# Optimization experiments

Measured on AMD Instinct MI355X. Metric: run time of the kernel, lower is better.

## Reference

```python
import jax, jax.numpy as jnp
import numpy as np

N = 1024          # num_features
H = N // 2        # core dimension (num_params // 2)
NB = 4            # num_blocks
B = 16384         # batch


def _lifted_core(rot_params, diag_params):
    """Build the (N, N) lifted core matrix for one Cayley block."""
    # skew-symmetric matrix from the H rotation params
    S = rot_params[:, None] - rot_params[None, :]            # (H, H)
    I = jnp.eye(H, dtype=rot_params.dtype)
    rotation = jnp.linalg.solve(I - S, I + S)                # Cayley transform
    core = diag_params[:, None] * rotation                   # diag(d) @ rotation
    # rot90(core, k=o) only depends on o mod 4 -> precompute 4 variants
    rots = jnp.stack([core,
                      jnp.rot90(core, 1),
                      jnp.rot90(core, 2),
                      jnp.rot90(core, 3)])                   # (4, H, H)

    def body(lifted, o):
        blk = jax.lax.dynamic_slice(lifted, (o, o), (H, H)) + rots[o % 4]
        return jax.lax.dynamic_update_slice(lifted, blk, (o, o)), None

    lifted, _ = jax.lax.scan(body, jnp.zeros((N, N), dtype=core.dtype),
                             jnp.arange(H + 1))
    return lifted


def setup_inputs() -> dict:
    key = jax.random.key(0)
    ks = jax.random.split(key, 5)
    x = jax.random.normal(ks[0], (B, N), dtype=jnp.float32)
    enc_rot = jax.random.normal(ks[1], (NB, H), dtype=jnp.float32)
    enc_diag = jax.random.normal(ks[2], (NB, H), dtype=jnp.float32)
    dec_rot = jax.random.normal(ks[3], (NB, H), dtype=jnp.float32)
    dec_diag = jax.random.normal(ks[4], (NB, H), dtype=jnp.float32)
    return {"x": x, "enc_rot": enc_rot, "enc_diag": enc_diag,
            "dec_rot": dec_rot, "dec_diag": dec_diag}


def reference(x, enc_rot, enc_diag, dec_rot, dec_diag):
    s = x
    for i in range(NB):                                      # encoder blocks
        s = s @ _lifted_core(enc_rot[i], enc_diag[i]).T
    bottleneck = s
    out = s
    for i in range(NB):                                      # decoder blocks
        out = out @ _lifted_core(dec_rot[i], dec_diag[i]).T
    return bottleneck, out
```

## Files before the change

kernel.cpp:

```cpp
#include <hip/hip_runtime.h>
#include <hip/hip_bf16.h>
#include <cstdint>
#include <cstddef>

#define H 512
#define NFEAT 1024
#define BATCH 16384
#define LM ((size_t)1 << 20)

using bf16 = __hip_bfloat16;
using bf16x8 = __attribute__((ext_vector_type(8))) __bf16;
using f32x4 = __attribute__((ext_vector_type(4))) float;
using f32x16 = __attribute__((ext_vector_type(16))) float;

__device__ __forceinline__ void gload16(void* lds, const void* g) {
  __builtin_amdgcn_global_load_lds(
      (__attribute__((address_space(1))) void*)g,
      (__attribute__((address_space(3))) void*)lds,
      16, 0, 0);
}

__global__ void prep_kernel(const float* __restrict__ er, const float* __restrict__ ed,
                            const float* __restrict__ dr, const float* __restrict__ dd,
                            float* __restrict__ ab) {
  const int mat = blockIdx.x;
  const int lane = threadIdx.x;
  const float* u = (mat < 4) ? (er + mat * H) : (dr + (mat - 4) * H);
  const float* d = (mat < 4) ? (ed + mat * H) : (dd + (mat - 4) * H);

  double s = 0.0, q = 0.0;
  for (int k = 0; k < 8; ++k) {
    double v = (double)u[lane + 64 * k];
    s += v;
    q += v * v;
  }
  for (int off = 32; off; off >>= 1) {
    s += __shfl_down(s, off);
    q += __shfl_down(q, off);
  }
  s = __shfl(s, 0);
  q = __shfl(q, 0);

  const double det = 1.0 - s * s + (double)H * q;
  const double cuv = 2.0 * (1.0 + s) / det;
  const double cuu = -2.0 * (double)H / det;
  const double cvv = -2.0 * q / det;
  const double cvu = -2.0 * (1.0 - s) / det;

  float* a = ab + mat * 1024;
  float* b = a + H;
  for (int k = 0; k < 8; ++k) {
    int idx = lane + 64 * k;
    double ui = (double)u[idx], di = (double)d[idx];
    a[idx] = (float)(di * (cuv * ui + cvv));
    b[idx] = (float)(di * (cuu * ui + cvu));
  }
}

__global__ __launch_bounds__(256) void prep2_kernel(
    const float* __restrict__ er, const float* __restrict__ ed,
    const float* __restrict__ dr, const float* __restrict__ dd,
    const float* __restrict__ ab, float* __restrict__ Tpref) {
  __shared__ float buf[4][512];
  __shared__ float tmp[4][512];
  const int mat = blockIdx.x;
  const float* d = (mat < 4) ? (ed + mat * H) : (dd + (mat - 4) * H);
  const float* a = ab + mat * 1024;
  const int t = threadIdx.x;
  for (int m = t; m < 512; m += 256) {
    buf[0][m] = a[m];
    buf[1][m] = a[511 - m];
    buf[2][m] = d[m];
    buf[3][m] = d[511 - m];
  }
  __syncthreads();
  for (int s = 4; s <= 256; s <<= 1) {
    for (int m = t; m < 512; m += 256)
#pragma unroll
      for (int q = 0; q < 4; ++q) tmp[q][m] = (m >= s) ? buf[q][m - s] : 0.f;
    __syncthreads();
    for (int m = t; m < 512; m += 256)
#pragma unroll
      for (int q = 0; q < 4; ++q) buf[q][m] += tmp[q][m];
    __syncthreads();
  }
  float* tp = Tpref + mat * 2048;
  for (int m = t; m < 512; m += 256) {
    tp[m] = buf[0][m];
    tp[512 + m] = buf[1][m];
    tp[1024 + m] = buf[2][m];
    tp[1536 + m] = buf[3][m];
  }
}

__global__ __launch_bounds__(256) void build_kernel(
    const float* __restrict__ er, const float* __restrict__ ed,
    const float* __restrict__ dr, const float* __restrict__ dd,
    const float* __restrict__ ab, const float* __restrict__ Tpref,
    bf16* __restrict__ Lbase) {
  __shared__ __align__(16) float arr4[4][520];
  __shared__ __align__(16) float4 up[132];
  __shared__ float pa[512], parev[512], pd[512], pdrev[512], sdl[512];

  const int i = blockIdx.x;
  const int mat = blockIdx.y;
  const float* u = (mat < 4) ? (er + mat * H) : (dr + (mat - 4) * H);
  const float* d = (mat < 4) ? (ed + mat * H) : (dd + (mat - 4) * H);
  const float* a = ab + mat * 1024;
  const float* b = a + H;
  const float* tp = Tpref + mat * 2048;
  const int t = threadIdx.x;

  for (int m = t; m < 520; m += 256) {
    arr4[0][m] = (m < 512) ? u[m] : 0.f;
    arr4[1][m] = (m >= 1 && m <= 512) ? b[m - 1] : 0.f;
    arr4[2][m] = (m >= 2 && m <= 513) ? u[513 - m] : 0.f;
    arr4[3][m] = (m >= 3 && m <= 514) ? b[514 - m] : 0.f;
  }
  for (int m = t; m < 512; m += 256) {
    pa[m] = tp[m];
    parev[m] = tp[512 + m];
    pd[m] = tp[1024 + m];
    pdrev[m] = tp[1536 + m];
    sdl[m] = d[m];
  }
  if (t < 132) {
    const int k4 = 4 * t;
    float4 v;
    int p0 = i - k4;
    v.x = (p0 >= 0 && p0 < 512) ? b[p0] : 0.f;
    int p1 = i - k4 - 1;
    v.y = (p1 >= 0 && p1 < 512) ? u[511 - p1] : 0.f;
    int p2 = i - k4 - 2;
    v.z = (p2 >= 0 && p2 < 512) ? b[511 - p2] : 0.f;
    int p3 = i - k4 - 3;
    v.w = (p3 >= 0 && p3 < 512) ? u[p3] : 0.f;
    up[t] = v;
  }
  __syncthreads();

  const float* upf = (const float*)up;
  const int j0 = t * 4;

  int lo_[4], hi_[4];
#pragma unroll
  for (int c = 0; c < 4; ++c) {
    const int jc = j0 + c;
    lo_[c] = max(0, max(i, jc) - 511);
    hi_[c] = min(512, min(i, jc));
  }
  const int CL = lo_[3];
  const int CH = hi_[0];

  float acc[4] = {0.f, 0.f, 0.f, 0.f};

#pragma unroll
  for (int c = 0; c < 4; ++c) {
    const int jc = j0 + c;
    const int lo = lo_[c], hi = hi_[c];
    if (lo > hi) continue;
    float v = 0.f;
    {
      int o1 = lo + ((0 - lo) & 3), o2 = hi - ((hi - 0) & 3);
      if (o1 <= o2) { int mx = i - o1, mn = i - o2; v += pa[mx] - (mn >= 4 ? pa[mn - 4] : 0.f); }
    }
    {
      int o1 = lo + ((1 - lo) & 3), o2 = hi - ((hi - 1) & 3);
      if (o1 <= o2) { int mx = jc - o1, mn = jc - o2; v += pa[mx] - (mn >= 4 ? pa[mn - 4] : 0.f); }
    }
    {
      int o1 = lo + ((2 - lo) & 3), o2 = hi - ((hi - 2) & 3);
      if (o1 <= o2) { int mx = i - o1, mn = i - o2; v += parev[mx] - (mn >= 4 ? parev[mn - 4] : 0.f); }
    }
    {
      int o1 = lo + ((3 - lo) & 3), o2 = hi - ((hi - 3) & 3);
      if (o1 <= o2) { int mx = jc - o1, mn = jc - o2; v += parev[mx] - (mn >= 4 ? parev[mn - 4] : 0.f); }
    }
    if (i == jc) {
      {
        int o1 = lo + ((0 - lo) & 3), o2 = hi - ((hi - 0) & 3);
        if (o1 <= o2) { int mx = i - o1, mn = i - o2; v += pd[mx] - (mn >= 4 ? pd[mn - 4] : 0.f); }
      }
      {
        int o1 = lo + ((2 - lo) & 3), o2 = hi - ((hi - 2) & 3);
        if (o1 <= o2) { int mx = i - o1, mn = i - o2; v += pdrev[mx] - (mn >= 4 ? pdrev[mn - 4] : 0.f); }
      }
    }
    const int m2 = i + jc - 511;
    if (m2 >= 0 && !(m2 & 1)) {
      const int os = m2 >> 1;
      if (os >= lo && os <= hi) {
        const int r = os & 3;
        if (r == 1) v += sdl[jc - os];
        else if (r == 3) v += sdl[511 - (jc - os)];
      }
    }
    acc[c] = v;
  }

  if (CL > CH) {
#pragma unroll
    for (int c = 0; c < 4; ++c) {
      const int jc = j0 + c;
      for (int o = lo_[c]; o <= hi_[c]; ++o) {
        const int r = o & 3;
        acc[c] += upf[o] * arr4[r][jc - o + r];
      }
    }
  } else {
#pragma unroll
    for (int c = 0; c < 4; ++c) {
      const int jc = j0 + c;
      const int he = min(hi_[c], CL - 1);
      for (int o = lo_[c]; o <= he; ++o) {
        const int r = o & 3;
        acc[c] += upf[o] * arr4[r][jc - o + r];
      }
      const int ls = max(lo_[c], CH + 1);
      for (int o = ls; o <= hi_[c]; ++o) {
        const int r = o & 3;
        acc[c] += upf[o] * arr4[r][jc - o + r];
      }
    }
    const int QL = (CL + 3) & ~3;
    for (int o = CL; o < QL && o <= CH; ++o) {
      const int r = o & 3;
      const float uvv = upf[o];
      const float4 wv = *(const float4*)&arr4[r][j0 - o + r];
      acc[0] += uvv * wv.x; acc[1] += uvv * wv.y;
      acc[2] += uvv * wv.z; acc[3] += uvv * wv.w;
    }
    int ob = QL;
    for (; ob + 3 <= CH; ob += 4) {
      const float4 uv = up[ob >> 2];
      const int x = j0 - ob;
      const float4 w0 = *(const float4*)&arr4[0][x];
      const float4 w1 = *(const float4*)&arr4[1][x];
      const float4 w2 = *(const float4*)&arr4[2][x];
      const float4 w3 = *(const float4*)&arr4[3][x];
      acc[0] += uv.x * w0.x + uv.y * w1.x + uv.z * w2.x + uv.w * w3.x;
      acc[1] += uv.x * w0.y + uv.y * w1.y + uv.z * w2.y + uv.w * w3.y;
      acc[2] += uv.x * w0.z + uv.y * w1.z + uv.z * w2.z + uv.w * w3.z;
      acc[3] += uv.x * w0.w + uv.y * w1.w + uv.z * w2.w + uv.w * w3.w;
    }
    for (int o = ob; o <= CH; ++o) {
      const int r = o & 3;
      const float uvv = upf[o];
      const float4 wv = *(const float4*)&arr4[r][j0 - o + r];
      acc[0] += uvv * wv.x; acc[1] += uvv * wv.y;
      acc[2] += uvv * wv.z; acc[3] += uvv * wv.w;
    }
  }

  const size_t off = ((size_t)mat << 21) + ((size_t)i << 10) + (size_t)j0;
  union { bf16 v[4]; ushort4 s; } Hu, Lu;
#pragma unroll
  for (int c = 0; c < 4; ++c) {
    const bf16 hb = __float2bfloat16(acc[c]);
    Hu.v[c] = hb;
    Lu.v[c] = __float2bfloat16(acc[c] - __bfloat162float(hb));
  }
  *(ushort4*)(Lbase + off) = Hu.s;
  *(ushort4*)(Lbase + off + LM) = Lu.s;
}

__global__ void splith_kernel(const float* __restrict__ x, bf16* __restrict__ h) {
  const int n4 = BATCH * NFEAT / 4;
  int idx = blockIdx.x * blockDim.x + threadIdx.x;
  int stride = gridDim.x * blockDim.x;
  for (int i = idx; i < n4; i += stride) {
    float4 v = ((const float4*)x)[i];
    union { bf16 b[4]; short4 s; } Hu;
    Hu.b[0] = __float2bfloat16(v.x);
    Hu.b[1] = __float2bfloat16(v.y);
    Hu.b[2] = __float2bfloat16(v.z);
    Hu.b[3] = __float2bfloat16(v.w);
    ((short4*)h)[i] = Hu.s;
  }
}

struct TPtrs { const bf16* s; bf16* d; };
struct T6 { TPtrs t[6]; };

__global__ __launch_bounds__(256) void transposeB_kernel(T6 p) {
  const bf16* S = p.t[blockIdx.z].s;
  bf16* D = p.t[blockIdx.z].d;
  __shared__ ushort tile[64][68];
  const int i0 = blockIdx.x * 64, j0 = blockIdx.y * 64;
  const int tid = threadIdx.x;
  const int rr = tid >> 4;
  const int cc = (tid & 15) * 4;
#pragma unroll
  for (int it = 0; it < 4; ++it) {
    const int row = it * 16 + rr;
    const size_t so = (size_t)(i0 + row) * 1024 + j0 + cc;
    ushort4 v = *(const ushort4*)((const ushort*)S + so);
    tile[row][cc] = v.x; tile[row][cc + 1] = v.y;
    tile[row][cc + 2] = v.z; tile[row][cc + 3] = v.w;
  }
  __syncthreads();
#pragma unroll
  for (int it = 0; it < 4; ++it) {
    const int row = it * 16 + rr;
    ushort4 o;
    o.x = tile[cc][row];     o.y = tile[cc + 1][row];
    o.z = tile[cc + 2][row]; o.w = tile[cc + 3][row];
    const size_t dofs = (size_t)(j0 + row) * 1024 + i0 + cc;
    *(ushort4*)((ushort*)D + dofs) = o;
  }
}

struct GPtrs { const bf16* a; const bf16* b; bf16* yh; bf16* yl; };
struct G4 { GPtrs g[4]; };

__global__ __launch_bounds__(256) void chaingemm4_kernel(G4 p) {
  GPtrs q = p.g[blockIdx.z];
  const bf16* A = q.a;
  const bf16* Bh = q.b;
  const bf16* Bl = q.b + LM;

  __shared__ __align__(16) bf16 smem[2 * 3 * 4096];

  const int tid = threadIdx.x;
  const int lane = tid & 63;
  const int wave = tid >> 6;
  const int wr = wave >> 1, wc = wave & 1;
  const int r0 = blockIdx.x * 64, c0 = blockIdx.y * 64;

  const int srow = tid >> 3;
  const int scol = (((tid & 7) ^ (srow & 7))) * 8;
  const int dst = tid * 8;
  const size_t ga0 = (size_t)(r0 + srow) * 1024 + scol;
  const size_t gb0 = (size_t)(c0 + srow) * 1024 + scol;

  auto STAGE = [&](int nb, int k0) {
    bf16* base = smem + nb * 12288;
    gload16(base + dst,        A + ga0 + k0);
    gload16(base + 2048 + dst, A + ga0 + 32 * 1024 + k0);
    gload16(base + 4096 + dst,        Bh + gb0 + k0);
    gload16(base + 4096 + 2048 + dst, Bh + gb0 + 32 * 1024 + k0);
    gload16(base + 8192 + dst,        Bl + gb0 + k0);
    gload16(base + 8192 + 2048 + dst, Bl + gb0 + 32 * 1024 + k0);
  };

  const int l31 = lane & 31;
  const int klg = lane >> 5;
  const int ar = wr * 32 + l31;
  const int br = wc * 32 + l31;
  int aoff[4], boff[4];
#pragma unroll
  for (int ks = 0; ks < 4; ++ks) {
    const int lgA = (ks << 1) | klg;
    aoff[ks] = ar * 64 + ((lgA ^ (ar & 7)) << 3);
    boff[ks] = br * 64 + ((lgA ^ (br & 7)) << 3);
  }

  f32x16 acc = {};

  STAGE(0, 0);
  asm volatile("s_waitcnt vmcnt(0)" ::: "memory");
  __builtin_amdgcn_s_barrier();

  for (int t = 0; t < 16; ++t) {
    const int buf = t & 1;
    const int nb = buf ^ 1;
    const bool pf = (t < 15);
    if (pf) STAGE(nb, (t + 1) * 64);

    const bf16* pA = smem + buf * 12288;
    const bf16* pBh = pA + 4096;
    const bf16* pBl = pA + 8192;
#pragma unroll
    for (int ks = 0; ks < 4; ++ks) {
      bf16x8 ah = *(const bf16x8*)(pA + aoff[ks]);
      bf16x8 bh = *(const bf16x8*)(pBh + boff[ks]);
      bf16x8 bl = *(const bf16x8*)(pBl + boff[ks]);
      acc = __builtin_amdgcn_mfma_f32_32x32x16_bf16(ah, bh, acc, 0, 0, 0);
      acc = __builtin_amdgcn_mfma_f32_32x32x16_bf16(ah, bl, acc, 0, 0, 0);
    }
    if (pf) asm volatile("s_waitcnt vmcnt(0)" ::: "memory");
    __builtin_amdgcn_s_barrier();
  }

  const int oc = c0 + wc * 32 + l31;
  const int rb = (lane >> 5) << 2;
#pragma unroll
  for (int r = 0; r < 16; ++r) {
    const int gr = r0 + wr * 32 + (r & 3) + ((r >> 2) << 3) + rb;
    const size_t off = (size_t)gr * 1024 + oc;
    const float v = acc[r];
    const bf16 hb = __float2bfloat16(v);
    q.yh[off] = hb;
    q.yl[off] = __float2bfloat16(v - __bfloat162float(hb));
  }
}

__global__ __launch_bounds__(512, 1) void gemmbig_kernel(
    const bf16* __restrict__ A, const bf16* __restrict__ Bh_,
    float* __restrict__ Y0, float* __restrict__ Y1) {
  __shared__ __align__(16) bf16 smem[2 * 2 * 8192];

  const int tid = threadIdx.x;
  const int lane = tid & 63;
  const int wave = tid >> 6;
  const int wr = wave >> 2;
  const int wc = wave & 3;

  const int pdisp = blockIdx.x + (blockIdx.y << 6);
  const int xcd = pdisp & 7;
  const int chk = pdisp >> 3;
  const int row0 = (xcd * 8 + (chk >> 3)) * 256;
  const int col0 = (chk & 7) * 256;

  const int gsrc = (tid & 3) ^ ((tid >> 3) & 3);
  const int dst = tid * 8;
  const size_t abase = (size_t)(row0 + (tid >> 2)) * NFEAT + gsrc * 8;
  const size_t bbase = (size_t)(col0 + (tid >> 2)) * NFEAT + gsrc * 8;

  auto STAGE2 = [&](int nb, int arr, const bf16* __restrict__ src, size_t base, int k0) {
    bf16* d = smem + nb * 16384 + arr * 8192 + dst;
    gload16(d, src + base + k0);
    gload16(d + 4096, src + base + 131072 + k0);
  };

  const int l31 = lane & 31;
  const int hb = lane >> 5;
  int aoffB[4][2], boffB[2][2];
#pragma unroll
  for (int m = 0; m < 4; ++m) {
    const int r = wr * 128 + m * 32 + l31;
#pragma unroll
    for (int ks = 0; ks < 2; ++ks)
      aoffB[m][ks] = r * 64 + ((((ks << 1) | hb) ^ ((r >> 1) & 3)) << 4);
  }
#pragma unroll
  for (int n = 0; n < 2; ++n) {
    const int r = wc * 64 + n * 32 + l31;
#pragma unroll
    for (int ks = 0; ks < 2; ++ks)
      boffB[n][ks] = r * 64 + ((((ks << 1) | hb) ^ ((r >> 1) & 3)) << 4);
  }

  auto LD = [](const char* base, int off) { return *(const bf16x8*)(base + off); };

  f32x16 acc[4][2] = {};

  STAGE2(0, 0, A, abase, 0);
  STAGE2(0, 1, Bh_, bbase, 0);
  asm volatile("s_waitcnt vmcnt(0)" ::: "memory");
  __builtin_amdgcn_s_barrier();

  for (int t = 0; t < 32; ++t) {
    const int buf = t & 1;
    const int nb = buf ^ 1;
    const int k1 = (t + 1) * 32;
    const char* pA = (const char*)(smem + buf * 16384);
    const char* pBh = pA + 16384;
    const bool pf = (t < 31);

    bf16x8 ga[2][2], fbh[2][2];

    if (pf) {
      STAGE2(nb, 0, A, abase, k1);
      STAGE2(nb, 1, Bh_, bbase, k1);
    }
#pragma unroll
    for (int mi = 0; mi < 2; ++mi)
#pragma unroll
      for (int ks = 0; ks < 2; ++ks)
        ga[mi][ks] = LD(pA, aoffB[mi][ks]);
#pragma unroll
    for (int n = 0; n < 2; ++n)
#pragma unroll
      for (int ks = 0; ks < 2; ++ks)
        fbh[n][ks] = LD(pBh, boffB[n][ks]);
    __builtin_amdgcn_s_barrier();
    __builtin_amdgcn_s_setprio(1);
#pragma unroll
    for (int ks = 0; ks < 2; ++ks)
#pragma unroll
      for (int mi = 0; mi < 2; ++mi)
#pragma unroll
        for (int n = 0; n < 2; ++n)
          acc[mi][n] = __builtin_amdgcn_mfma_f32_32x32x16_bf16(ga[mi][ks], fbh[n][ks], acc[mi][n], 0, 0, 0);
    __builtin_amdgcn_s_setprio(0);
    __builtin_amdgcn_s_barrier();

#pragma unroll
    for (int mi = 0; mi < 2; ++mi)
#pragma unroll
      for (int ks = 0; ks < 2; ++ks)
        ga[mi][ks] = LD(pA, aoffB[2 + mi][ks]);
    __builtin_amdgcn_s_barrier();
    __builtin_amdgcn_s_setprio(1);
#pragma unroll
    for (int ks = 0; ks < 2; ++ks)
#pragma unroll
      for (int mi = 0; mi < 2; ++mi)
#pragma unroll
        for (int n = 0; n < 2; ++n)
          acc[2 + mi][n] = __builtin_amdgcn_mfma_f32_32x32x16_bf16(ga[mi][ks], fbh[n][ks], acc[2 + mi][n], 0, 0, 0);
    __builtin_amdgcn_s_setprio(0);
    if (pf) asm volatile("s_waitcnt vmcnt(0)" ::: "memory");
    __builtin_amdgcn_s_barrier();
  }

  float* Yb = (col0 < 1024) ? Y0 : (Y1 - 1024);
  const int ocol0 = col0 + wc * 64 + l31;
  const int rb = (lane >> 5) << 2;
#pragma unroll
  for (int m = 0; m < 4; ++m)
#pragma unroll
    for (int n = 0; n < 2; ++n)
#pragma unroll
      for (int r = 0; r < 16; ++r) {
        const int grow = row0 + wr * 128 + m * 32 + (r & 3) + ((r >> 2) << 3) + rb;
        const int gcol = ocol0 + n * 32;
        Yb[(size_t)grow * NFEAT + (size_t)gcol] = acc[m][n][r];
      }
}

extern "C" void kernel_launch(void* const* d_in, const int* in_sizes, int n_in,
                              void* d_out, int out_size, void* d_ws, size_t ws_size,
                              hipStream_t stream) {
  (void)in_sizes; (void)n_in; (void)out_size; (void)ws_size;
  const float* x  = (const float*)d_in[0];
  const float* er = (const float*)d_in[1];
  const float* ed = (const float*)d_in[2];
  const float* dr = (const float*)d_in[3];
  const float* dd = (const float*)d_in[4];

  float* O0 = (float*)d_out;
  float* O1 = O0 + (size_t)BATCH * NFEAT;

  bf16* Lb = (bf16*)d_ws;
  float* ab = (float*)(Lb + 16 * LM);
  bf16* Qh = (bf16*)(ab + 8 * 1024);

  float* Tpref = O0;
  bf16* SB = (bf16*)((char*)O0 + (1 << 20));
  auto slot = [&](int s) { return SB + (size_t)s * LM; };

  prep_kernel<<<8, 64, 0, stream>>>(er, ed, dr, dd, ab);
  prep2_kernel<<<8, 256, 0, stream>>>(er, ed, dr, dd, ab, Tpref);
  build_kernel<<<dim3(1024, 8), 256, 0, stream>>>(er, ed, dr, dd, ab, Tpref, Lb);
  splith_kernel<<<4096, 256, 0, stream>>>(x, Qh);

  {
    T6 p;
    p.t[0] = {Lb + 0 * LM,  slot(0)};
    p.t[1] = {Lb + 4 * LM,  slot(2)};
    p.t[2] = {Lb + 5 * LM,  slot(3)};
    p.t[3] = {Lb + 8 * LM,  slot(4)};
    p.t[4] = {Lb + 12 * LM, slot(6)};
    p.t[5] = {Lb + 13 * LM, slot(7)};
    transposeB_kernel<<<dim3(16, 16, 6), 256, 0, stream>>>(p);
  }
  {
    G4 p;
    p.g[0] = {slot(0),      Lb + 2 * LM,  slot(8),  slot(9)};
    p.g[1] = {Lb + 6 * LM,  slot(2),      slot(10), slot(11)};
    p.g[2] = {slot(4),      Lb + 10 * LM, slot(12), slot(13)};
    p.g[3] = {Lb + 14 * LM, slot(6),      slot(14), slot(15)};
    chaingemm4_kernel<<<dim3(16, 16, 4), 256, 0, stream>>>(p);
  }
  {
    G4 p;
    p.g[0] = {slot(8),  slot(10), slot(0), slot(1)};
    p.g[1] = {slot(12), slot(14), slot(2), slot(3)};
    p.g[2] = p.g[0];
    p.g[3] = p.g[1];
    chaingemm4_kernel<<<dim3(16, 16, 2), 256, 0, stream>>>(p);
  }
  {
    T6 p;
    p.t[0] = {slot(0), Lb + 0 * LM};
    p.t[1] = {slot(2), Lb + 2 * LM};
    p.t[2] = p.t[0]; p.t[3] = p.t[0]; p.t[4] = p.t[0]; p.t[5] = p.t[0];
    transposeB_kernel<<<dim3(16, 16, 2), 256, 0, stream>>>(p);
  }
  {
    G4 p;
    p.g[0] = {Lb + 2 * LM, slot(0), Lb + 1 * LM, slot(4)};
    p.g[1] = p.g[0]; p.g[2] = p.g[0]; p.g[3] = p.g[0];
    chaingemm4_kernel<<<dim3(16, 16, 1), 256, 0, stream>>>(p);
  }

  gemmbig_kernel<<<dim3(64, 8), 512, 0, stream>>>(Qh, Lb, O0, O1);
}
```

Baseline: 279.7 us.

## Recast lifted-matrix build as split-bf16 MFMA GEMM over generated operands

Replaces the scalar per-row build kernel, which summed the banded rank-style contributions with FP32 FMAs, with two stages. The first writes per-matrix A/B operand panels (K=576) split into bf16 high and low parts. The second multiplies them with 32x32x16 bf16 MFMA using three products (hh, hl, lh) to keep near-FP32 accuracy, then adds the closed-form prefix-sum terms before emitting hi/lo bf16 outputs. This moves the O(N^3) build work onto matrix cores, at the cost of extra operand traffic through the O1 scratch area and narrow 2-byte scattered stores in the epilogue.

Result: faster. 259.3 us (-7.3%).

```diff
diff --git a/kernel.cpp b/kernel.cpp
--- a/kernel.cpp
+++ b/kernel.cpp
@@ -7,6 +7,7 @@
 #define NFEAT 1024
 #define BATCH 16384
 #define LM ((size_t)1 << 20)
+#define KOP 576
 
 using bf16 = __hip_bfloat16;
 using bf16x8 = __attribute__((ext_vector_type(8))) __bf16;
@@ -93,80 +94,147 @@
   }
 }
 
-__global__ __launch_bounds__(256) void build_kernel(
-    const float* __restrict__ er, const float* __restrict__ ed,
-    const float* __restrict__ dr, const float* __restrict__ dd,
-    const float* __restrict__ ab, const float* __restrict__ Tpref,
-    bf16* __restrict__ Lbase) {
-  __shared__ __align__(16) float arr4[4][520];
-  __shared__ __align__(16) float4 up[132];
-  __shared__ float pa[512], parev[512], pd[512], pdrev[512], sdl[512];
-
-  const int i = blockIdx.x;
+__global__ __launch_bounds__(256) void genops_kernel(
+    const float* __restrict__ er, const float* __restrict__ dr,
+    const float* __restrict__ ab,
+    bf16* __restrict__ Ah, bf16* __restrict__ Al,
+    bf16* __restrict__ Bh, bf16* __restrict__ Bl) {
+  const int x = blockIdx.x;
   const int mat = blockIdx.y;
   const float* u = (mat < 4) ? (er + mat * H) : (dr + (mat - 4) * H);
-  const float* d = (mat < 4) ? (ed + mat * H) : (dd + (mat - 4) * H);
-  const float* a = ab + mat * 1024;
-  const float* b = a + H;
-  const float* tp = Tpref + mat * 2048;
+  const float* b = ab + mat * 1024 + H;
   const int t = threadIdx.x;
-
-  for (int m = t; m < 520; m += 256) {
-    arr4[0][m] = (m < 512) ? u[m] : 0.f;
-    arr4[1][m] = (m >= 1 && m <= 512) ? b[m - 1] : 0.f;
-    arr4[2][m] = (m >= 2 && m <= 513) ? u[513 - m] : 0.f;
-    arr4[3][m] = (m >= 3 && m <= 514) ? b[514 - m] : 0.f;
-  }
-  for (int m = t; m < 512; m += 256) {
-    pa[m] = tp[m];
-    parev[m] = tp[512 + m];
-    pd[m] = tp[1024 + m];
-    pdrev[m] = tp[1536 + m];
-    sdl[m] = d[m];
-  }
-  if (t < 132) {
-    const int k4 = 4 * t;
-    float4 v;
-    int p0 = i - k4;
-    v.x = (p0 >= 0 && p0 < 512) ? b[p0] : 0.f;
-    int p1 = i - k4 - 1;
-    v.y = (p1 >= 0 && p1 < 512) ? u[511 - p1] : 0.f;
-    int p2 = i - k4 - 2;
-    v.z = (p2 >= 0 && p2 < 512) ? b[511 - p2] : 0.f;
-    int p3 = i - k4 - 3;
-    v.w = (p3 >= 0 && p3 < 512) ? u[p3] : 0.f;
-    up[t] = v;
-  }
-  __syncthreads();
-
-  const float* upf = (const float*)up;
-  const int j0 = t * 4;
-
-  int lo_[4], hi_[4];
-#pragma unroll
-  for (int c = 0; c < 4; ++c) {
-    const int jc = j0 + c;
-    lo_[c] = max(0, max(i, jc) - 511);
-    hi_[c] = min(512, min(i, jc));
-  }
-  const int CL = lo_[3];
-  const int CH = hi_[0];
-
-  float acc[4] = {0.f, 0.f, 0.f, 0.f};
-
-#pragma unroll
-  for (int c = 0; c < 4; ++c) {
-    const int jc = j0 + c;
-    const int lo = lo_[c], hi = hi_[c];
-    if (lo > hi) continue;
+  const size_t base = ((size_t)mat * 1024 + x) * KOP;
+  for (int k = t; k < KOP; k += 256) {
+    float av = 0.f, bv = 0.f;
+    if (k <= 128) {
+      const int o = 4 * k;
+      const int ia = x - o;
+      av = (ia >= 0 && ia < 512) ? b[ia] : 0.f;
+      bv = (ia >= 0 && ia < 512) ? u[ia] : 0.f;
+    } else if (k <= 256) {
+      const int o = 4 * (k - 129) + 1;
+      const int ia = 511 - x + o;
+      const int ib = x - o;
+      av = (ia >= 0 && ia < 512) ? u[ia] : 0.f;
+      bv = (ib >= 0 && ib < 512) ? b[ib] : 0.f;
+    } else if (k <= 384) {
+      const int o = 4 * (k - 257) + 2;
+      const int ia = 511 - x + o;
+      av = (ia >= 0 && ia < 512) ? b[ia] : 0.f;
+      bv = (ia >= 0 && ia < 512) ? u[ia] : 0.f;
+    } else if (k <= 512) {
+      const int o = 4 * (k - 385) + 3;
+      const int ia = x - o;
+      const int ib = 511 - x + o;
+      av = (ia >= 0 && ia < 512) ? u[ia] : 0.f;
+      bv = (ib >= 0 && ib < 512) ? b[ib] : 0.f;
+    }
+    const bf16 ah = __float2bfloat16(av);
+    Ah[base + k] = ah;
+    Al[base + k] = __float2bfloat16(av - __bfloat162float(ah));
+    const bf16 bh = __float2bfloat16(bv);
+    Bh[base + k] = bh;
+    Bl[base + k] = __float2bfloat16(bv - __bfloat162float(bh));
+  }
+}
+
+__global__ __launch_bounds__(256) void buildgemm_kernel(
+    const bf16* __restrict__ Ah, const bf16* __restrict__ Al,
+    const bf16* __restrict__ Bh, const bf16* __restrict__ Bl,
+    const float* __restrict__ ed, const float* __restrict__ dd,
+    const float* __restrict__ Tpref, bf16* __restrict__ Lbase) {
+  __shared__ __align__(16) bf16 smem[4 * 8192];
+  __shared__ float pa[512], parev[512], pd[512], pdrev[512], sdl[512];
+  bf16* sAh = smem;
+  bf16* sAl = smem + 8192;
+  bf16* sBh = smem + 16384;
+  bf16* sBl = smem + 24576;
+
+  const int tid = threadIdx.x;
+  const int lane = tid & 63;
+  const int wave = tid >> 6;
+  const int wr = wave >> 1;
+  const int wc = wave & 1;
+  const int mat = blockIdx.z;
+  const int row0 = blockIdx.x * 128;
+  const int col0 = blockIdx.y * 128;
+
+  {
+    const float* tp = Tpref + mat * 2048;
+    const float* d = (mat < 4) ? (ed + mat * H) : (dd + (mat - 4) * H);
+    for (int m = tid; m < 512; m += 256) {
+      pa[m] = tp[m];
+      parev[m] = tp[512 + m];
+      pd[m] = tp[1024 + m];
+      pdrev[m] = tp[1536 + m];
+      sdl[m] = d[m];
+    }
+  }
+
+  const size_t OPS = (size_t)mat * 1024 * KOP;
+  const int srow = tid >> 3;
+  const int sce = (((tid * 16) ^ (((tid >> 3) & 7) << 4)) & 127) >> 1;
+  const size_t abase = OPS + (size_t)(row0 + srow) * KOP + sce;
+  const size_t bbase = OPS + (size_t)(col0 + srow) * KOP + sce;
+  const int dst0 = tid * 8;
+
+  f32x16 acc[2][2] = {};
+
+  for (int kt = 0; kt < 9; ++kt) {
+    const int k0 = kt * 64;
+#pragma unroll
+    for (int q = 0; q < 4; ++q) {
+      const size_t ga = abase + (size_t)(32 * q) * KOP + k0;
+      const size_t gb = bbase + (size_t)(32 * q) * KOP + k0;
+      const int dq = q * 2048 + dst0;
+      gload16(sAh + dq, Ah + ga);
+      gload16(sAl + dq, Al + ga);
+      gload16(sBh + dq, Bh + gb);
+      gload16(sBl + dq, Bl + gb);
+    }
+    __syncthreads();
+
+    const int l31 = lane & 31;
+    const int kh16 = (lane >> 5) * 16;
+#pragma unroll
+    for (int ks = 0; ks < 4; ++ks) {
+      bf16x8 fah[2], fal[2], fbh[2], fbl[2];
+#pragma unroll
+      for (int m = 0; m < 2; ++m) {
+        const int arow = wr * 64 + m * 32 + l31;
+        const int abk = (arow * 128 + ks * 32 + kh16) ^ ((arow & 7) << 4);
+        fah[m] = *(const bf16x8*)((const char*)sAh + abk);
+        fal[m] = *(const bf16x8*)((const char*)sAl + abk);
+        const int brow = wc * 64 + m * 32 + l31;
+        const int bbk = (brow * 128 + ks * 32 + kh16) ^ ((brow & 7) << 4);
+        fbh[m] = *(const bf16x8*)((const char*)sBh + bbk);
+        fbl[m] = *(const bf16x8*)((const char*)sBl + bbk);
+      }
+#pragma unroll
+      for (int m = 0; m < 2; ++m)
+#pragma unroll
+        for (int n = 0; n < 2; ++n) {
+          acc[m][n] = __builtin_amdgcn_mfma_f32_32x32x16_bf16(fah[m], fbh[n], acc[m][n], 0, 0, 0);
+          acc[m][n] = __builtin_amdgcn_mfma_f32_32x32x16_bf16(fah[m], fbl[n], acc[m][n], 0, 0, 0);
+          acc[m][n] = __builtin_amdgcn_mfma_f32_32x32x16_bf16(fal[m], fbh[n], acc[m][n], 0, 0, 0);
+        }
+    }
+    __syncthreads();
+  }
+
+  auto apart = [&](int i, int j) -> float {
+    const int lo = max(0, max(i, j) - 511);
+    const int hi = min(512, min(i, j));
+    if (lo > hi) return 0.f;
     float v = 0.f;
     {
-      int o1 = lo + ((0 - lo) & 3), o2 = hi - ((hi - 0) & 3);
+      int o1 = lo + ((0 - lo) & 3), o2 = hi - (hi & 3);
       if (o1 <= o2) { int mx = i - o1, mn = i - o2; v += pa[mx] - (mn >= 4 ? pa[mn - 4] : 0.f); }
     }
     {
       int o1 = lo + ((1 - lo) & 3), o2 = hi - ((hi - 1) & 3);
-      if (o1 <= o2) { int mx = jc - o1, mn = jc - o2; v += pa[mx] - (mn >= 4 ? pa[mn - 4] : 0.f); }
+      if (o1 <= o2) { int mx = j - o1, mn = j - o2; v += pa[mx] - (mn >= 4 ? pa[mn - 4] : 0.f); }
     }
     {
       int o1 = lo + ((2 - lo) & 3), o2 = hi - ((hi - 2) & 3);
@@ -174,11 +242,11 @@
     }
     {
       int o1 = lo + ((3 - lo) & 3), o2 = hi - ((hi - 3) & 3);
-      if (o1 <= o2) { int mx = jc - o1, mn = jc - o2; v += parev[mx] - (mn >= 4 ? parev[mn - 4] : 0.f); }
-    }
-    if (i == jc) {
+      if (o1 <= o2) { int mx = j - o1, mn = j - o2; v += parev[mx] - (mn >= 4 ? parev[mn - 4] : 0.f); }
+    }
+    if (i == j) {
       {
-        int o1 = lo + ((0 - lo) & 3), o2 = hi - ((hi - 0) & 3);
+        int o1 = lo + ((0 - lo) & 3), o2 = hi - (hi & 3);
         if (o1 <= o2) { int mx = i - o1, mn = i - o2; v += pd[mx] - (mn >= 4 ? pd[mn - 4] : 0.f); }
       }
       {
@@ -186,82 +254,34 @@
         if (o1 <= o2) { int mx = i - o1, mn = i - o2; v += pdrev[mx] - (mn >= 4 ? pdrev[mn - 4] : 0.f); }
       }
     }
-    const int m2 = i + jc - 511;
+    const int m2 = i + j - 511;
     if (m2 >= 0 && !(m2 & 1)) {
       const int os = m2 >> 1;
       if (os >= lo && os <= hi) {
         const int r = os & 3;
-        if (r == 1) v += sdl[jc - os];
-        else if (r == 3) v += sdl[511 - (jc - os)];
+        if (r == 1) v += sdl[j - os];
+        else if (r == 3) v += sdl[511 - (j - os)];
       }
     }
-    acc[c] = v;
-  }
-
-  if (CL > CH) {
-#pragma unroll
-    for (int c = 0; c < 4; ++c) {
-      const int jc = j0 + c;
-      for (int o = lo_[c]; o <= hi_[c]; ++o) {
-        const int r = o & 3;
-        acc[c] += upf[o] * arr4[r][jc - o + r];
+    return v;
+  };
+
+  const int ocol0 = col0 + wc * 64 + (lane & 31);
+  const int rb = (lane >> 5) << 2;
+#pragma unroll
+  for (int m = 0; m < 2; ++m)
+#pragma unroll
+    for (int n = 0; n < 2; ++n)
+#pragma unroll
+      for (int r = 0; r < 16; ++r) {
+        const int grow = row0 + wr * 64 + m * 32 + (r & 3) + ((r >> 2) << 3) + rb;
+        const int gcol = ocol0 + n * 32;
+        const float v = acc[m][n][r] + apart(grow, gcol);
+        const size_t off = ((size_t)mat << 21) + ((size_t)grow << 10) + (size_t)gcol;
+        const bf16 hb = __float2bfloat16(v);
+        Lbase[off] = hb;
+        Lbase[off + LM] = __float2bfloat16(v - __bfloat162float(hb));
       }
-    }
-  } else {
-#pragma unroll
-    for (int c = 0; c < 4; ++c) {
-      const int jc = j0 + c;
-      const int he = min(hi_[c], CL - 1);
-      for (int o = lo_[c]; o <= he; ++o) {
-        const int r = o & 3;
-        acc[c] += upf[o] * arr4[r][jc - o + r];
-      }
-      const int ls = max(lo_[c], CH + 1);
-      for (int o = ls; o <= hi_[c]; ++o) {
-        const int r = o & 3;
-        acc[c] += upf[o] * arr4[r][jc - o + r];
-      }
-    }
-    const int QL = (CL + 3) & ~3;
-    for (int o = CL; o < QL && o <= CH; ++o) {
-      const int r = o & 3;
-      const float uvv = upf[o];
-      const float4 wv = *(const float4*)&arr4[r][j0 - o + r];
-      acc[0] += uvv * wv.x; acc[1] += uvv * wv.y;
-      acc[2] += uvv * wv.z; acc[3] += uvv * wv.w;
-    }
-    int ob = QL;
-    for (; ob + 3 <= CH; ob += 4) {
-      const float4 uv = up[ob >> 2];
-      const int x = j0 - ob;
-      const float4 w0 = *(const float4*)&arr4[0][x];
-      const float4 w1 = *(const float4*)&arr4[1][x];
-      const float4 w2 = *(const float4*)&arr4[2][x];
-      const float4 w3 = *(const float4*)&arr4[3][x];
-      acc[0] += uv.x * w0.x + uv.y * w1.x + uv.z * w2.x + uv.w * w3.x;
-      acc[1] += uv.x * w0.y + uv.y * w1.y + uv.z * w2.y + uv.w * w3.y;
-      acc[2] += uv.x * w0.z + uv.y * w1.z + uv.z * w2.z + uv.w * w3.z;
-      acc[3] += uv.x * w0.w + uv.y * w1.w + uv.z * w2.w + uv.w * w3.w;
-    }
-    for (int o = ob; o <= CH; ++o) {
-      const int r = o & 3;
-      const float uvv = upf[o];
-      const float4 wv = *(const float4*)&arr4[r][j0 - o + r];
-      acc[0] += uvv * wv.x; acc[1] += uvv * wv.y;
-      acc[2] += uvv * wv.z; acc[3] += uvv * wv.w;
-    }
-  }
-
-  const size_t off = ((size_t)mat << 21) + ((size_t)i << 10) + (size_t)j0;
-  union { bf16 v[4]; ushort4 s; } Hu, Lu;
-#pragma unroll
-  for (int c = 0; c < 4; ++c) {
-    const bf16 hb = __float2bfloat16(acc[c]);
-    Hu.v[c] = hb;
-    Lu.v[c] = __float2bfloat16(acc[c] - __bfloat162float(hb));
-  }
-  *(ushort4*)(Lbase + off) = Hu.s;
-  *(ushort4*)(Lbase + off + LM) = Lu.s;
 }
 
 __global__ void splith_kernel(const float* __restrict__ x, bf16* __restrict__ h) {
@@ -541,9 +561,17 @@
   bf16* SB = (bf16*)((char*)O0 + (1 << 20));
   auto slot = [&](int s) { return SB + (size_t)s * LM; };
 
+  const size_t OPN = (size_t)8 * 1024 * KOP;
+  bf16* Aoph = (bf16*)O1;
+  bf16* Aopl = Aoph + OPN;
+  bf16* Boph = Aopl + OPN;
+  bf16* Bopl = Boph + OPN;
+
   prep_kernel<<<8, 64, 0, stream>>>(er, ed, dr, dd, ab);
   prep2_kernel<<<8, 256, 0, stream>>>(er, ed, dr, dd, ab, Tpref);
-  build_kernel<<<dim3(1024, 8), 256, 0, stream>>>(er, ed, dr, dd, ab, Tpref, Lb);
+  genops_kernel<<<dim3(1024, 8), 256, 0, stream>>>(er, dr, ab, Aoph, Aopl, Boph, Bopl);
+  buildgemm_kernel<<<dim3(8, 8, 8), 256, 0, stream>>>(Aoph, Aopl, Boph, Bopl,
+                                                      ed, dd, Tpref, Lb);
   splith_kernel<<<4096, 256, 0, stream>>>(x, Qh);
 
   {
```
